# Performance work log

Hardware: AMD Instinct MI355X
Metric: run time of the kernel (lower is better)

Reference implementation:

```python
import jax, jax.numpy as jnp
import numpy as np

N_NODES = 100000
N_EDGES = 1600000


def setup_inputs() -> dict:
    key = jax.random.key(0)
    k1, k2, k3, k4, k5, k6 = jax.random.split(key, 6)
    x = jax.random.normal(k1, (N_NODES, 2), dtype=jnp.float32)
    edge_index = jax.random.randint(k2, (2, N_EDGES), 0, N_NODES, dtype=jnp.int64)
    # Glorot-style init for GCN weights, zeros for biases (PyG defaults)
    W1 = jax.random.normal(k3, (2, 64), dtype=jnp.float32) * (1.0 / np.sqrt(2.0))
    b1 = jnp.zeros((64,), dtype=jnp.float32)
    W2 = jax.random.normal(k4, (64, 1), dtype=jnp.float32) * (1.0 / np.sqrt(64.0))
    b2 = jnp.zeros((1,), dtype=jnp.float32)
    return {"x": x, "edge_index": edge_index, "W1": W1, "b1": b1, "W2": W2, "b2": b2}


def reference(x, edge_index, W1, b1, W2, b2):
    N = x.shape[0]
    row, col = edge_index[0], edge_index[1]  # source, target (PyG flow source_to_target)
    # symmetric GCN normalization, degrees from target index (no self loops)
    deg = jax.ops.segment_sum(jnp.ones(edge_index.shape[1], x.dtype), col, num_segments=N)
    deg_inv_sqrt = jnp.where(deg > 0, jnp.where(deg > 0, deg, 1.0) ** -0.5, 0.0)
    norm = (deg_inv_sqrt[row] * deg_inv_sqrt[col])[:, None]  # [E,1]

    def gcn_conv(h, W, b):
        h = h @ W                       # [N,F_out] tiny GEMM
        msg = h[row] * norm             # gather + scale: [E,F_out]
        agg = jax.ops.segment_sum(msg, col, num_segments=N)  # scatter-add
        return agg + b

    h = jax.nn.relu(gcn_conv(x, W1, b1))   # dropout is identity in eval mode
    out = jax.nn.relu(gcn_conv(h, W2, b2))
    return out
```

## Files before the change

### kernel.cpp

```cpp
#include <hip/hip_runtime.h>
#include <math.h>

#define NN 100000
#define NE 1600000
#define BKT 391
#define NB 256
#define EPB 6400
#define NPB 250
#define STRIDE 7168
#define RT 1024

__global__ void __launch_bounds__(RT) reorder_kernel(
        const int* __restrict__ row, const int* __restrict__ col,
        unsigned* __restrict__ cursor, unsigned* __restrict__ packed) {
    __shared__ int h[NB], lb[NB];
    __shared__ unsigned gaddr[NB], glim[NB];
    __shared__ int wsum[RT / 64];
    __shared__ uint2 sga[EPB];
    const int t = threadIdx.x;
    const int lane = t & 63, wid = t >> 6;
    const int e0 = blockIdx.x * EPB;

    for (int i = t; i < NB; i += RT) h[i] = 0;
    __syncthreads();

    const int4* rv = (const int4*)(row + e0);
    const int4* cv = (const int4*)(col + e0);
    unsigned pk[8]; int bb[8];
#pragma unroll
    for (int u = 0; u < 8; ++u) bb[u] = -1;
#pragma unroll
    for (int g = 0; g < 2; ++g) {
        int grp = g * RT + t;
        if (grp < EPB / 4) {
            int4 r4 = rv[grp], c4 = cv[grp];
            int rr[4] = {r4.x, r4.y, r4.z, r4.w};
            int cc[4] = {c4.x, c4.y, c4.z, c4.w};
#pragma unroll
            for (int j = 0; j < 4; ++j) {
                int b = cc[j] / BKT;
                int cl = cc[j] - b * BKT;
                pk[4 * g + j] = ((unsigned)rr[j] << 9) | (unsigned)cl;
                bb[4 * g + j] = b;
            }
        }
    }
#pragma unroll
    for (int u = 0; u < 8; ++u)
        if (bb[u] >= 0) atomicAdd(&h[bb[u]], 1);
    __syncthreads();

    int v = (t < NB) ? h[t] : 0;
    int incl = v;
#pragma unroll
    for (int d = 1; d < 64; d <<= 1) {
        int u2 = __shfl_up(incl, d);
        if (lane >= d) incl += u2;
    }
    if (lane == 63) wsum[wid] = incl;
    __syncthreads();
    int off = 0;
#pragma unroll
    for (int j = 0; j < 3; ++j)
        if (j < wid) off += wsum[j];
    if (t < NB) {
        lb[t] = off + incl - v;
        unsigned base = v ? atomicAdd(&cursor[t], (unsigned)v) : 0u;
        gaddr[t] = (unsigned)t * STRIDE + base;
        glim[t]  = (unsigned)(t + 1) * STRIDE;
    }
    __syncthreads();
    for (int i = t; i < NB; i += RT) h[i] = 0;
    __syncthreads();

#pragma unroll
    for (int u = 0; u < 8; ++u) {
        if (bb[u] >= 0) {
            int b = bb[u];
            int r = atomicAdd(&h[b], 1);
            unsigned a = gaddr[b] + (unsigned)r;
            if (a >= glim[b]) a = 0xFFFFFFFFu;
            sga[lb[b] + r] = make_uint2(pk[u], a);
        }
    }
    __syncthreads();
    for (int i = t; i < EPB; i += RT) {
        uint2 e = sga[i];
        if (e.y != 0xFFFFFFFFu) packed[e.y] = e.x;
    }
}

__global__ void __launch_bounds__(RT) degscan_kernel(
        const unsigned* __restrict__ packed, const unsigned* __restrict__ cursor,
        const float2* __restrict__ x2,
        float2* __restrict__ y2, unsigned* __restrict__ rng32) {
    __shared__ int cnt[BKT];
    __shared__ int wsum[(BKT + 63) / 64];
    const int t = threadIdx.x;
    const int lane = t & 63, wid = t >> 6;
    const int b = blockIdx.x;
    const unsigned s0 = (unsigned)b * STRIDE;
    const int L = min((int)cursor[b], STRIDE);
    const int L4 = L >> 2;

    for (int i = t; i < BKT; i += RT) cnt[i] = 0;
    __syncthreads();

    const uint4* pv4 = (const uint4*)(packed + s0);
    for (int g = t; g < L4; g += RT) {
        uint4 p4 = pv4[g];
        atomicAdd(&cnt[p4.x & 511u], 1);
        atomicAdd(&cnt[p4.y & 511u], 1);
        atomicAdd(&cnt[p4.z & 511u], 1);
        atomicAdd(&cnt[p4.w & 511u], 1);
    }
    for (int i = 4 * L4 + t; i < L; i += RT)
        atomicAdd(&cnt[packed[s0 + i] & 511u], 1);
    __syncthreads();

    int v = (t < BKT) ? cnt[t] : 0;
    int incl = v;
#pragma unroll
    for (int d = 1; d < 64; d <<= 1) {
        int u2 = __shfl_up(incl, d);
        if (lane >= d) incl += u2;
    }
    if (lane == 63 && wid < (BKT + 63) / 64) wsum[wid] = incl;
    __syncthreads();
    int off = 0;
#pragma unroll
    for (int j = 0; j < (BKT + 63) / 64 - 1; ++j)
        if (j < wid) off += wsum[j];
    if (t < BKT) {
        int sex = off + incl - v;
        int node = b * BKT + t;
        if (node < NN) {
            float dv = (v > 0) ? rsqrtf((float)v) : 0.0f;
            float2 xv = x2[node];
            y2[node] = make_float2(xv.x * dv, xv.y * dv);
            rng32[node] = ((unsigned)sex << 16) | (unsigned)v;
        }
    }
}

__global__ void __launch_bounds__(RT) sortconv1_kernel(
        const unsigned* __restrict__ packed, const unsigned* __restrict__ cursor,
        const float2* __restrict__ y2, const unsigned* __restrict__ rng32,
        const float* __restrict__ W1, const float* __restrict__ b1,
        const float* __restrict__ W2,
        unsigned* __restrict__ srow, float* __restrict__ z2) {
    __shared__ int rk[BKT], sexA[BKT], cntA[BKT];
    __shared__ float sW0[64], sW1[64], sb1[64], sW2[64];
    __shared__ unsigned srt[STRIDE];
    const int t = threadIdx.x;
    const int b = blockIdx.x;
    const unsigned s0 = (unsigned)b * STRIDE;
    const int L = min((int)cursor[b], STRIDE);
    const int L4 = L >> 2;

    if (t < 64) { sW0[t] = W1[t]; sW1[t] = W1[64 + t]; sb1[t] = b1[t]; sW2[t] = W2[t]; }
    for (int i = t; i < BKT; i += RT) rk[i] = 0;
    if (t < BKT) {
        int node = b * BKT + t;
        unsigned u = (node < NN) ? rng32[node] : 0u;
        sexA[t] = (int)(u >> 16);
        cntA[t] = (int)(u & 0xFFFFu);
    }
    __syncthreads();

    const uint4* pv4 = (const uint4*)(packed + s0);
    for (int g = t; g < L4; g += RT) {
        uint4 p4 = pv4[g];
        unsigned pp[4] = {p4.x, p4.y, p4.z, p4.w};
#pragma unroll
        for (int j = 0; j < 4; ++j) {
            int cl = pp[j] & 511u;
            int r = atomicAdd(&rk[cl], 1);
            srt[sexA[cl] + r] = pp[j] >> 9;
        }
    }
    for (int i = 4 * L4 + t; i < L; i += RT) {
        unsigned p = packed[s0 + i];
        int cl = p & 511u;
        int r = atomicAdd(&rk[cl], 1);
        srt[sexA[cl] + r] = p >> 9;
    }
    __syncthreads();

    uint4* so4 = (uint4*)(srow + s0);
    for (int g = t; g < L4; g += RT) so4[g] = ((const uint4*)srt)[g];
    for (int i = 4 * L4 + t; i < L; i += RT) srow[s0 + i] = srt[i];

    const int tau = t >> 1, par = t & 1;
    if (t < 2 * BKT) {
        int start = sexA[tau], deg = cntA[tau];
        float sx = 0.f, sy = 0.f;
        for (int k = start + par; k < start + deg; k += 2) {
            float2 w = y2[srt[k]];
            sx += w.x; sy += w.y;
        }
        sx += __shfl_xor(sx, 1); sy += __shfl_xor(sy, 1);
        float dv = (deg > 0) ? rsqrtf((float)deg) : 0.0f;
        float a0 = sx * dv, a1 = sy * dv;
        float acc = 0.0f;
        int j0 = par * 32;
#pragma unroll
        for (int jj = 0; jj < 32; ++jj) {
            int j = j0 + jj;
            float h = fmaf(a0, sW0[j], fmaf(a1, sW1[j], sb1[j]));
            acc = fmaf(fmaxf(h, 0.0f), sW2[j], acc);
        }
        acc += __shfl_xor(acc, 1);
        int node = b * BKT + tau;
        if (par == 0 && node < NN) z2[node] = acc * dv;
    }
}

__global__ void conv2_kernel(const unsigned* __restrict__ srow, const unsigned* __restrict__ rng32,
                             const float* __restrict__ z2,
                             const float* __restrict__ b2, float* __restrict__ out) {
    int t = threadIdx.x;
    int lane = t & 3;
    int node = blockIdx.x * 64 + (t >> 2);
    if (node >= NN) return;
    unsigned u = rng32[node];
    int bk = node / BKT;
    unsigned start = (unsigned)bk * STRIDE + (u >> 16);
    int deg = (int)(u & 0xFFFFu);
    float s = 0.f;
    for (unsigned k = start + lane; k < start + (unsigned)deg; k += 4)
        s += z2[srow[k]];
    s += __shfl_xor(s, 1);
    s += __shfl_xor(s, 2);
    if (lane == 0) {
        float dv = (deg > 0) ? rsqrtf((float)deg) : 0.0f;
        out[node] = fmaxf(fmaf(dv, s, b2[0]), 0.0f);
    }
}

extern "C" void kernel_launch(void* const* d_in, const int* in_sizes, int n_in,
                              void* d_out, int out_size, void* d_ws, size_t ws_size,
                              hipStream_t stream) {
    const float* x  = (const float*)d_in[0];
    const int*   ei = (const int*)d_in[1];
    const float* W1 = (const float*)d_in[2];
    const float* b1 = (const float*)d_in[3];
    const float* W2 = (const float*)d_in[4];
    const float* b2 = (const float*)d_in[5];
    float* out = (float*)d_out;

    const int* row = ei;
    const int* col = ei + NE;

    unsigned* packed = (unsigned*)d_ws;
    unsigned* srow   = packed + (size_t)NB * STRIDE;
    float2*   y2     = (float2*)(srow + (size_t)NB * STRIDE);
    float*    z2     = (float*)(y2 + NN);
    unsigned* rng32  = (unsigned*)(z2 + NN);
    unsigned* cursor = rng32 + NN;

    hipMemsetAsync(cursor, 0, NB * sizeof(unsigned), stream);

    reorder_kernel  <<<NPB, RT, 0, stream>>>(row, col, cursor, packed);
    degscan_kernel  <<<NB, RT, 0, stream>>>(packed, cursor, (const float2*)x, y2, rng32);
    sortconv1_kernel<<<NB, RT, 0, stream>>>(packed, cursor, (const float2*)y2, rng32,
                                            W1, b1, W2, srow, z2);
    conv2_kernel    <<<(NN + 63) / 64, 256, 0, stream>>>(srow, rng32, z2, b2, out);
}
```

Baseline: 110.2 us.

## Replace global atomic bucket cursors with fixed per-chunk slots and count table

Each reorder block now writes its bucket entries into a fixed slot of CSUB entries per (bucket, chunk) pair and records per-chunk counts in a table. This replaces the global atomicAdd cursors and the memset. Downstream kernels read the count table and stream the slots with masking. This removes the global atomics and the memset launch, and makes write positions deterministic. In exchange, the packed buffer is larger and sparse, so reads take more masked work, and any chunk with more than CSUB edges in a bucket silently drops those edges.

```diff
diff --git a/kernel.cpp b/kernel.cpp
--- a/kernel.cpp
+++ b/kernel.cpp
@@ -7,19 +7,22 @@
 #define NB 256
 #define EPB 6400
 #define NPB 250
-#define STRIDE 7168
+#define CSUB 80
+#define GPC (CSUB / 4)
+#define BSTRIDE (NPB * CSUB)
+#define SST 7168
 #define RT 1024
 
 __global__ void __launch_bounds__(RT) reorder_kernel(
         const int* __restrict__ row, const int* __restrict__ col,
-        unsigned* __restrict__ cursor, unsigned* __restrict__ packed) {
+        unsigned* __restrict__ cnt_bc, unsigned* __restrict__ packed) {
     __shared__ int h[NB], lb[NB];
-    __shared__ unsigned gaddr[NB], glim[NB];
     __shared__ int wsum[RT / 64];
     __shared__ uint2 sga[EPB];
     const int t = threadIdx.x;
     const int lane = t & 63, wid = t >> 6;
-    const int e0 = blockIdx.x * EPB;
+    const int c = blockIdx.x;
+    const int e0 = c * EPB;
 
     for (int i = t; i < NB; i += RT) h[i] = 0;
     __syncthreads();
@@ -51,6 +54,7 @@
     __syncthreads();
 
     int v = (t < NB) ? h[t] : 0;
+    if (t < NB) cnt_bc[(unsigned)c * NB + t] = (unsigned)v;
     int incl = v;
 #pragma unroll
     for (int d = 1; d < 64; d <<= 1) {
@@ -63,12 +67,7 @@
 #pragma unroll
     for (int j = 0; j < 3; ++j)
         if (j < wid) off += wsum[j];
-    if (t < NB) {
-        lb[t] = off + incl - v;
-        unsigned base = v ? atomicAdd(&cursor[t], (unsigned)v) : 0u;
-        gaddr[t] = (unsigned)t * STRIDE + base;
-        glim[t]  = (unsigned)(t + 1) * STRIDE;
-    }
+    if (t < NB) lb[t] = off + incl - v;
     __syncthreads();
     for (int i = t; i < NB; i += RT) h[i] = 0;
     __syncthreads();
@@ -78,8 +77,8 @@
         if (bb[u] >= 0) {
             int b = bb[u];
             int r = atomicAdd(&h[b], 1);
-            unsigned a = gaddr[b] + (unsigned)r;
-            if (a >= glim[b]) a = 0xFFFFFFFFu;
+            unsigned a = (unsigned)b * BSTRIDE + (unsigned)c * CSUB + (unsigned)r;
+            if (r >= CSUB) a = 0xFFFFFFFFu;
             sga[lb[b] + r] = make_uint2(pk[u], a);
         }
     }
@@ -90,32 +89,39 @@
     }
 }
 
+#define MASKED_STREAM(PROCESS)                                              \
+    for (int g = t; g < NPB * GPC; g += RT) {                               \
+        int c_ = g / GPC;                                                   \
+        int k_ = (g - c_ * GPC) * 4;                                        \
+        int n_ = scnt[c_];                                                  \
+        if (k_ < n_) {                                                      \
+            uint4 p4 = *(const uint4*)(packed + base + c_ * CSUB + k_);     \
+            PROCESS(p4.x);                                                  \
+            if (k_ + 1 < n_) { PROCESS(p4.y); }                             \
+            if (k_ + 2 < n_) { PROCESS(p4.z); }                             \
+            if (k_ + 3 < n_) { PROCESS(p4.w); }                             \
+        }                                                                   \
+    }
+
 __global__ void __launch_bounds__(RT) degscan_kernel(
-        const unsigned* __restrict__ packed, const unsigned* __restrict__ cursor,
+        const unsigned* __restrict__ packed, const unsigned* __restrict__ cnt_bc,
         const float2* __restrict__ x2,
         float2* __restrict__ y2, unsigned* __restrict__ rng32) {
     __shared__ int cnt[BKT];
+    __shared__ int scnt[NPB];
     __shared__ int wsum[(BKT + 63) / 64];
     const int t = threadIdx.x;
     const int lane = t & 63, wid = t >> 6;
     const int b = blockIdx.x;
-    const unsigned s0 = (unsigned)b * STRIDE;
-    const int L = min((int)cursor[b], STRIDE);
-    const int L4 = L >> 2;
+    const unsigned base = (unsigned)b * BSTRIDE;
 
     for (int i = t; i < BKT; i += RT) cnt[i] = 0;
-    __syncthreads();
-
-    const uint4* pv4 = (const uint4*)(packed + s0);
-    for (int g = t; g < L4; g += RT) {
-        uint4 p4 = pv4[g];
-        atomicAdd(&cnt[p4.x & 511u], 1);
-        atomicAdd(&cnt[p4.y & 511u], 1);
-        atomicAdd(&cnt[p4.z & 511u], 1);
-        atomicAdd(&cnt[p4.w & 511u], 1);
-    }
-    for (int i = 4 * L4 + t; i < L; i += RT)
-        atomicAdd(&cnt[packed[s0 + i] & 511u], 1);
+    if (t < NPB) scnt[t] = (int)cnt_bc[(unsigned)t * NB + b];
+    __syncthreads();
+
+#define HISTP(w) atomicAdd(&cnt[(w) & 511u], 1)
+    MASKED_STREAM(HISTP)
+#undef HISTP
     __syncthreads();
 
     int v = (t < BKT) ? cnt[t] : 0;
@@ -144,22 +150,24 @@
 }
 
 __global__ void __launch_bounds__(RT) sortconv1_kernel(
-        const unsigned* __restrict__ packed, const unsigned* __restrict__ cursor,
+        const unsigned* __restrict__ packed, const unsigned* __restrict__ cnt_bc,
         const float2* __restrict__ y2, const unsigned* __restrict__ rng32,
         const float* __restrict__ W1, const float* __restrict__ b1,
         const float* __restrict__ W2,
         unsigned* __restrict__ srow, float* __restrict__ z2) {
     __shared__ int rk[BKT], sexA[BKT], cntA[BKT];
+    __shared__ int scnt[NPB];
+    __shared__ int LtotS;
     __shared__ float sW0[64], sW1[64], sb1[64], sW2[64];
-    __shared__ unsigned srt[STRIDE];
+    __shared__ unsigned srt[SST];
     const int t = threadIdx.x;
     const int b = blockIdx.x;
-    const unsigned s0 = (unsigned)b * STRIDE;
-    const int L = min((int)cursor[b], STRIDE);
-    const int L4 = L >> 2;
+    const unsigned base = (unsigned)b * BSTRIDE;
 
     if (t < 64) { sW0[t] = W1[t]; sW1[t] = W1[64 + t]; sb1[t] = b1[t]; sW2[t] = W2[t]; }
+    if (t == 0) LtotS = 0;
     for (int i = t; i < BKT; i += RT) rk[i] = 0;
+    if (t < NPB) scnt[t] = (int)cnt_bc[(unsigned)t * NB + b];
     if (t < BKT) {
         int node = b * BKT + t;
         unsigned u = (node < NN) ? rng32[node] : 0u;
@@ -167,29 +175,19 @@
         cntA[t] = (int)(u & 0xFFFFu);
     }
     __syncthreads();
-
-    const uint4* pv4 = (const uint4*)(packed + s0);
-    for (int g = t; g < L4; g += RT) {
-        uint4 p4 = pv4[g];
-        unsigned pp[4] = {p4.x, p4.y, p4.z, p4.w};
-#pragma unroll
-        for (int j = 0; j < 4; ++j) {
-            int cl = pp[j] & 511u;
-            int r = atomicAdd(&rk[cl], 1);
-            srt[sexA[cl] + r] = pp[j] >> 9;
-        }
-    }
-    for (int i = 4 * L4 + t; i < L; i += RT) {
-        unsigned p = packed[s0 + i];
-        int cl = p & 511u;
-        int r = atomicAdd(&rk[cl], 1);
-        srt[sexA[cl] + r] = p >> 9;
-    }
-    __syncthreads();
-
-    uint4* so4 = (uint4*)(srow + s0);
+    if (t < NPB) atomicAdd(&LtotS, scnt[t]);
+
+#define SCATP(w) { int cl_ = (w) & 511u; int r_ = atomicAdd(&rk[cl_], 1); \
+                   srt[sexA[cl_] + r_] = (w) >> 9; }
+    MASKED_STREAM(SCATP)
+#undef SCATP
+    __syncthreads();
+
+    const int Ltot = LtotS;
+    const int L4 = Ltot >> 2;
+    uint4* so4 = (uint4*)(srow + (unsigned)b * SST);
     for (int g = t; g < L4; g += RT) so4[g] = ((const uint4*)srt)[g];
-    for (int i = 4 * L4 + t; i < L; i += RT) srow[s0 + i] = srt[i];
+    for (int i = 4 * L4 + t; i < Ltot; i += RT) srow[(unsigned)b * SST + i] = srt[i];
 
     const int tau = t >> 1, par = t & 1;
     if (t < 2 * BKT) {
@@ -225,7 +223,7 @@
     if (node >= NN) return;
     unsigned u = rng32[node];
     int bk = node / BKT;
-    unsigned start = (unsigned)bk * STRIDE + (u >> 16);
+    unsigned start = (unsigned)bk * SST + (u >> 16);
     int deg = (int)(u & 0xFFFFu);
     float s = 0.f;
     for (unsigned k = start + lane; k < start + (unsigned)deg; k += 4)
@@ -253,17 +251,15 @@
     const int* col = ei + NE;
 
     unsigned* packed = (unsigned*)d_ws;
-    unsigned* srow   = packed + (size_t)NB * STRIDE;
-    float2*   y2     = (float2*)(srow + (size_t)NB * STRIDE);
+    unsigned* cnt_bc = packed + (size_t)NB * BSTRIDE;
+    unsigned* srow   = cnt_bc + (size_t)NPB * NB;
+    float2*   y2     = (float2*)(srow + (size_t)NB * SST);
     float*    z2     = (float*)(y2 + NN);
     unsigned* rng32  = (unsigned*)(z2 + NN);
-    unsigned* cursor = rng32 + NN;
-
-    hipMemsetAsync(cursor, 0, NB * sizeof(unsigned), stream);
-
-    reorder_kernel  <<<NPB, RT, 0, stream>>>(row, col, cursor, packed);
-    degscan_kernel  <<<NB, RT, 0, stream>>>(packed, cursor, (const float2*)x, y2, rng32);
-    sortconv1_kernel<<<NB, RT, 0, stream>>>(packed, cursor, (const float2*)y2, rng32,
+
+    reorder_kernel  <<<NPB, RT, 0, stream>>>(row, col, cnt_bc, packed);
+    degscan_kernel  <<<NB, RT, 0, stream>>>(packed, cnt_bc, (const float2*)x, y2, rng32);
+    sortconv1_kernel<<<NB, RT, 0, stream>>>(packed, cnt_bc, (const float2*)y2, rng32,
                                             W1, b1, W2, srow, z2);
     conv2_kernel    <<<(NN + 63) / 64, 256, 0, stream>>>(srow, rng32, z2, b2, out);
 }
```

Result: no change. 110.1 us (-0.0%).
